# Optimization experiments

Measured on AMD Instinct MI355X. Metric: run time of the kernel, lower is better.

Reference implementation:

```python
import jax, jax.numpy as jnp
import numpy as np


def setup_inputs() -> dict:
    key = jax.random.key(0)
    ks = jax.random.split(key, 8)
    B, H, W, D, U = 128, 16, 48, 512, 512
    s = 1.0 / np.sqrt(D)
    return {
        "dec_hidden": jax.random.normal(ks[0], (B, D), jnp.float32),
        "enc_output": jax.random.normal(ks[1], (B, H, W, D), jnp.float32),
        "W1_w": jax.random.normal(ks[2], (D, U), jnp.float32) * s,
        "W1_b": jnp.zeros((U,), jnp.float32),
        "W2_w": jax.random.normal(ks[3], (D, U), jnp.float32) * s,
        "W2_b": jnp.zeros((U,), jnp.float32),
        "V_w": jax.random.normal(ks[4], (U, 1), jnp.float32) * (1.0 / np.sqrt(U)),
        "V_b": jnp.zeros((1,), jnp.float32),
    }


def reference(dec_hidden, enc_output, W1_w, W1_b, W2_w, W2_b, V_w, V_b):
    # dec_hidden: [B, Dd] -> [B, 1, 1, Dd]
    dec = dec_hidden[:, None, None, :]
    # W1(enc_output): [B, H, W, U]; W2(dec): [B, 1, 1, U] (broadcast add)
    h = jnp.tanh(jnp.einsum('bhwd,du->bhwu', enc_output, W1_w) + W1_b
                 + (dec @ W2_w + W2_b))
    # V(.) -> score [B, H, W, 1]
    score = jnp.einsum('bhwu,uo->bhwo', h, V_w) + V_b
    # softmax over axis=1 (H axis), matching tf.keras softmax(score, axis=1)
    attention_weights = jax.nn.softmax(score, axis=1)
    # context: sum over spatial axes -> [B, D]
    context_vector = jnp.sum(attention_weights * enc_output, axis=(1, 2))
    return context_vector, attention_weights
```

## Files before the change

kernel.cpp:

```cpp
#include <hip/hip_runtime.h>
#include <hip/hip_bf16.h>

typedef __attribute__((ext_vector_type(8))) short short8;
typedef __attribute__((ext_vector_type(4))) float f32x4;
typedef unsigned short ushort;

#define BB 128
#define HHH 16
#define WWW 48
#define DD 512
#define UU 512
#define ROWS_PER_B (HHH * WWW)
#define MTOT (BB * ROWS_PER_B)

__device__ __forceinline__ ushort f2bf(float f) {
    unsigned int u = __float_as_uint(f);
    u += 0x7fffu + ((u >> 16) & 1u);
    return (ushort)(u >> 16);
}

__device__ __forceinline__ void gload_lds16(const ushort* g, ushort* l) {
    __builtin_amdgcn_global_load_lds(
        (const __attribute__((address_space(1))) unsigned int*)(const void*)g,
        (__attribute__((address_space(3))) unsigned int*)(void*)l,
        16, 0, 0);
}

__global__ __launch_bounds__(256) void pack_w1p_kernel(const float* __restrict__ w1,
                                                       ushort* __restrict__ w1p) {
    __shared__ __align__(16) ushort tile[64 * 72];
    const int t  = threadIdx.x;
    const int u0 = blockIdx.x * 64;
    const int kc = blockIdx.y;
    const int ul = t & 63;
    const int db = t >> 6;
#pragma unroll
    for (int i = 0; i < 16; ++i) {
        const int d = db + i * 4;
        tile[ul * 72 + d] = f2bf(w1[(size_t)(kc * 64 + d) * UU + u0 + ul]);
    }
    __syncthreads();
    const int u = t >> 2;
    const int s = (t & 3) * 2;
    const int x = u & 7;
    short8 v0 = *(const short8*)&tile[u * 72 + s * 8];
    short8 v1 = *(const short8*)&tile[u * 72 + s * 8 + 8];
    *(short8*)&w1p[(size_t)kc * 32768 + (u0 + u) * 64 + (( s      ^ x)) * 8] = v0;
    *(short8*)&w1p[(size_t)kc * 32768 + (u0 + u) * 64 + (((s + 1) ^ x)) * 8] = v1;
}

__global__ __launch_bounds__(256) void dproj_kernel(
        const float* __restrict__ dec, const float* __restrict__ w2,
        const float* __restrict__ w1b, const float* __restrict__ w2b,
        float* __restrict__ dproj) {
    const int b = blockIdx.y;
    const int u = blockIdx.x * 256 + threadIdx.x;
    float acc = 0.f;
#pragma unroll 8
    for (int d = 0; d < DD; ++d)
        acc += dec[b * DD + d] * w2[(size_t)d * UU + u];
    dproj[b * UU + u] = acc + w1b[u] + w2b[u];
}

__global__ __launch_bounds__(512, 2) void score_kernel(
        const float* __restrict__ enc, const ushort* __restrict__ w1p,
        const float* __restrict__ dproj, const float* __restrict__ vw,
        const float* __restrict__ vb, float* __restrict__ score) {
    __shared__ __align__(16) ushort Bb[2][512 * 64];
    __shared__ __align__(16) ushort Ab[128 * 64];

    const int tid  = threadIdx.x;
    const int lane = tid & 63;
    const int wave = tid >> 6;
    const int mbase = blockIdx.x * 128;
    const int b = mbase / ROWS_PER_B;

    const int mh   = wave >> 2;
    const int uc   = wave & 3;
    const int lrow = lane & 15;
    const int kgrp = lane >> 4;

    const int ar  = tid >> 2;
    const int asp = (tid & 3) * 2;
    const float* abase = enc + (size_t)(mbase + ar) * DD + asp * 8;
    const int s0p = ( asp      ^ (ar & 7)) * 8;
    const int s1p = ((asp + 1) ^ (ar & 7)) * 8;

    f32x4 acc[4][8] = {};

    {
        float4 a0 = ((const float4*)abase)[0];
        float4 a1 = ((const float4*)abase)[1];
        float4 a2 = ((const float4*)abase)[2];
        float4 a3 = ((const float4*)abase)[3];
        const ushort* bsrc = w1p + tid * 8;
#pragma unroll
        for (int i = 0; i < 8; ++i)
            gload_lds16(bsrc + i * 4096, &Bb[0][tid * 8 + i * 4096]);
        short8 w0, w1v;
        ushort* p0 = (ushort*)&w0; ushort* p1 = (ushort*)&w1v;
        p0[0]=f2bf(a0.x); p0[1]=f2bf(a0.y); p0[2]=f2bf(a0.z); p0[3]=f2bf(a0.w);
        p0[4]=f2bf(a1.x); p0[5]=f2bf(a1.y); p0[6]=f2bf(a1.z); p0[7]=f2bf(a1.w);
        p1[0]=f2bf(a2.x); p1[1]=f2bf(a2.y); p1[2]=f2bf(a2.z); p1[3]=f2bf(a2.w);
        p1[4]=f2bf(a3.x); p1[5]=f2bf(a3.y); p1[6]=f2bf(a3.z); p1[7]=f2bf(a3.w);
        *(short8*)&Ab[ar * 64 + s0p] = w0;
        *(short8*)&Ab[ar * 64 + s1p] = w1v;
    }

    int cur = 0;
    for (int kc = 0; kc < 8; ++kc) {
        __syncthreads();

        float4 a0, a1, a2, a3;
        if (kc < 7) {
            const float* asrc = abase + (kc + 1) * 64;
            a0 = ((const float4*)asrc)[0];
            a1 = ((const float4*)asrc)[1];
            a2 = ((const float4*)asrc)[2];
            a3 = ((const float4*)asrc)[3];
            const ushort* bsrc = w1p + (size_t)(kc + 1) * 32768 + tid * 8;
#pragma unroll
            for (int i = 0; i < 8; ++i)
                gload_lds16(bsrc + i * 4096, &Bb[cur ^ 1][tid * 8 + i * 4096]);
        }

        const ushort* Bc = &Bb[cur][0];
#pragma unroll
        for (int kk = 0; kk < 2; ++kk) {
            const int sub = kk * 4 + kgrp;
            short8 a[4], bf[8];
#pragma unroll
            for (int ms = 0; ms < 4; ++ms) {
                const int r = mh * 64 + ms * 16 + lrow;
                a[ms] = *(const short8*)&Ab[r * 64 + (sub ^ (r & 7)) * 8];
            }
#pragma unroll
            for (int uf = 0; uf < 8; ++uf) {
                const int u = uc * 128 + uf * 16 + lrow;
                bf[uf] = *(const short8*)&Bc[u * 64 + (sub ^ (u & 7)) * 8];
            }
#pragma unroll
            for (int ms = 0; ms < 4; ++ms)
#pragma unroll
                for (int uf = 0; uf < 8; ++uf)
                    acc[ms][uf] = __builtin_amdgcn_mfma_f32_16x16x32_bf16(
                        a[ms], bf[uf], acc[ms][uf], 0, 0, 0);
        }

        __syncthreads();

        if (kc < 7) {
            short8 w0, w1v;
            ushort* p0 = (ushort*)&w0; ushort* p1 = (ushort*)&w1v;
            p0[0]=f2bf(a0.x); p0[1]=f2bf(a0.y); p0[2]=f2bf(a0.z); p0[3]=f2bf(a0.w);
            p0[4]=f2bf(a1.x); p0[5]=f2bf(a1.y); p0[6]=f2bf(a1.z); p0[7]=f2bf(a1.w);
            p1[0]=f2bf(a2.x); p1[1]=f2bf(a2.y); p1[2]=f2bf(a2.z); p1[3]=f2bf(a2.w);
            p1[4]=f2bf(a3.x); p1[5]=f2bf(a3.y); p1[6]=f2bf(a3.z); p1[7]=f2bf(a3.w);
            *(short8*)&Ab[ar * 64 + s0p] = w0;
            *(short8*)&Ab[ar * 64 + s1p] = w1v;
        }
        cur ^= 1;
    }

    float part[4][4] = {};
#pragma unroll
    for (int uf = 0; uf < 8; ++uf) {
        const int u = uc * 128 + uf * 16 + lrow;
        const float cadd = dproj[b * UU + u];
        const float vwe  = vw[u];
#pragma unroll
        for (int ms = 0; ms < 4; ++ms)
#pragma unroll
            for (int j = 0; j < 4; ++j) {
                float x = acc[ms][uf][j] + cadd;
                x = fminf(fmaxf(x, -15.f), 15.f);
                float e = __expf(2.f * x);
                part[ms][j] += vwe * ((e - 1.f) / (e + 1.f));
            }
    }
#pragma unroll
    for (int off = 1; off < 16; off <<= 1)
#pragma unroll
        for (int ms = 0; ms < 4; ++ms)
#pragma unroll
            for (int j = 0; j < 4; ++j)
                part[ms][j] += __shfl_xor(part[ms][j], off, 64);

    float* scr = (float*)Ab;
    if (lrow == 0) {
#pragma unroll
        for (int ms = 0; ms < 4; ++ms)
#pragma unroll
            for (int j = 0; j < 4; ++j)
                scr[uc * 128 + mh * 64 + ms * 16 + kgrp * 4 + j] = part[ms][j];
    }
    __syncthreads();
    if (tid < 128)
        score[mbase + tid] = scr[tid] + scr[128 + tid] + scr[256 + tid]
                           + scr[384 + tid] + vb[0];
}

__global__ void softmax_kernel(const float* __restrict__ score,
                               float* __restrict__ attn) {
    const int g = blockIdx.x * blockDim.x + threadIdx.x;
    if (g >= BB * WWW) return;
    const int b = g / WWW, w = g % WWW;
    const float* s = score + b * ROWS_PER_B + w;
    float v[16];
    float m = -1e30f;
#pragma unroll
    for (int h = 0; h < HHH; ++h) { v[h] = s[h * WWW]; m = fmaxf(m, v[h]); }
    float sum = 0.f;
#pragma unroll
    for (int h = 0; h < HHH; ++h) { v[h] = __expf(v[h] - m); sum += v[h]; }
    const float inv = 1.f / sum;
    float* o = attn + b * ROWS_PER_B + w;
#pragma unroll
    for (int h = 0; h < HHH; ++h) o[h * WWW] = v[h] * inv;
}

__global__ __launch_bounds__(512) void ctx_partial_kernel(
        const float* __restrict__ enc, const float* __restrict__ attn,
        float* __restrict__ partial) {
    const int c = blockIdx.x;
    const int b = blockIdx.y;
    const int t = threadIdx.x;
    const int d4 = (t & 127) * 4;
    const int ro = t >> 7;
    float4 acc = {0.f, 0.f, 0.f, 0.f};
    const int rbase = c * 192;
#pragma unroll 8
    for (int i = 0; i < 48; ++i) {
        const int r = rbase + ro + i * 4;
        const float a = attn[b * ROWS_PER_B + r];
        const float4 e = *(const float4*)(enc + ((size_t)(b * ROWS_PER_B + r)) * DD + d4);
        acc.x += a * e.x; acc.y += a * e.y; acc.z += a * e.z; acc.w += a * e.w;
    }
    *(float4*)(partial + ((size_t)((b * 4 + c) * 4 + ro)) * DD + d4) = acc;
}

__global__ void ctx_reduce_kernel(const float* __restrict__ partial,
                                  float* __restrict__ out) {
    const int q = blockIdx.x * 256 + threadIdx.x;
    const int b = q >> 7;
    const int d4 = (q & 127) * 4;
    float4 s = {0.f, 0.f, 0.f, 0.f};
#pragma unroll
    for (int j = 0; j < 16; ++j) {
        const float4 p = *(const float4*)(partial + ((size_t)(b * 16 + j)) * DD + d4);
        s.x += p.x; s.y += p.y; s.z += p.z; s.w += p.w;
    }
    *(float4*)(out + (size_t)b * DD + d4) = s;
}

extern "C" void kernel_launch(void* const* d_in, const int* in_sizes, int n_in,
                              void* d_out, int out_size, void* d_ws, size_t ws_size,
                              hipStream_t stream) {
    const float* dec = (const float*)d_in[0];
    const float* enc = (const float*)d_in[1];
    const float* w1w = (const float*)d_in[2];
    const float* w1b = (const float*)d_in[3];
    const float* w2w = (const float*)d_in[4];
    const float* w2b = (const float*)d_in[5];
    const float* vw  = (const float*)d_in[6];
    const float* vb  = (const float*)d_in[7];

    float* out = (float*)d_out;
    char* ws = (char*)d_ws;
    ushort* w1p    = (ushort*)(ws);
    float* dproj   = (float*)(ws + 524288);
    float* score   = (float*)(ws + 524288 + 262144);
    float* partial = (float*)(ws + 524288 + 262144 + 393216);

    float* ctx  = out;
    float* attn = out + BB * DD;

    pack_w1p_kernel<<<dim3(8, 8), 256, 0, stream>>>(w1w, w1p);
    dproj_kernel<<<dim3(2, BB), 256, 0, stream>>>(dec, w2w, w1b, w2b, dproj);
    score_kernel<<<MTOT / 128, 512, 0, stream>>>(enc, w1p, dproj, vw, vb, score);
    softmax_kernel<<<(BB * WWW + 255) / 256, 256, 0, stream>>>(score, attn);
    ctx_partial_kernel<<<dim3(4, BB), 512, 0, stream>>>(enc, attn, partial);
    ctx_reduce_kernel<<<64, 256, 0, stream>>>(partial, ctx);
}
```

Measured before the change: 409.0 us.

## Fuse prep and softmax kernels, double-buffer A tile to drop a barrier

Merges the W1 packing and decoder-projection kernels into one launch. Fuses the softmax into the context-partial kernel, which now recomputes softmax per batch from scores held in LDS and uses two row halves per batch instead of four. In the score GEMM, the A tile is double-buffered so the second __syncthreads per K step can be removed. This cuts launch overhead and barrier stalls, but raises LDS use to about 160KB per block and gives the context pass fewer blocks to work with.

```diff
diff --git a/kernel.cpp b/kernel.cpp
--- a/kernel.cpp
+++ b/kernel.cpp
@@ -26,48 +26,49 @@
         16, 0, 0);
 }
 
-__global__ __launch_bounds__(256) void pack_w1p_kernel(const float* __restrict__ w1,
-                                                       ushort* __restrict__ w1p) {
-    __shared__ __align__(16) ushort tile[64 * 72];
-    const int t  = threadIdx.x;
-    const int u0 = blockIdx.x * 64;
-    const int kc = blockIdx.y;
-    const int ul = t & 63;
-    const int db = t >> 6;
-#pragma unroll
-    for (int i = 0; i < 16; ++i) {
-        const int d = db + i * 4;
-        tile[ul * 72 + d] = f2bf(w1[(size_t)(kc * 64 + d) * UU + u0 + ul]);
-    }
-    __syncthreads();
-    const int u = t >> 2;
-    const int s = (t & 3) * 2;
-    const int x = u & 7;
-    short8 v0 = *(const short8*)&tile[u * 72 + s * 8];
-    short8 v1 = *(const short8*)&tile[u * 72 + s * 8 + 8];
-    *(short8*)&w1p[(size_t)kc * 32768 + (u0 + u) * 64 + (( s      ^ x)) * 8] = v0;
-    *(short8*)&w1p[(size_t)kc * 32768 + (u0 + u) * 64 + (((s + 1) ^ x)) * 8] = v1;
-}
-
-__global__ __launch_bounds__(256) void dproj_kernel(
-        const float* __restrict__ dec, const float* __restrict__ w2,
-        const float* __restrict__ w1b, const float* __restrict__ w2b,
-        float* __restrict__ dproj) {
-    const int b = blockIdx.y;
-    const int u = blockIdx.x * 256 + threadIdx.x;
-    float acc = 0.f;
+__global__ __launch_bounds__(256) void prep_kernel(
+        const float* __restrict__ w1, const float* __restrict__ dec,
+        const float* __restrict__ w2, const float* __restrict__ w1b,
+        const float* __restrict__ w2b,
+        ushort* __restrict__ w1p, float* __restrict__ dproj) {
+    const int t = threadIdx.x;
+    if (blockIdx.x < 64) {
+        __shared__ __align__(16) ushort tile[64 * 72];
+        const int u0 = (blockIdx.x & 7) * 64;
+        const int kc = blockIdx.x >> 3;
+        const int ul = t & 63;
+        const int db = t >> 6;
+#pragma unroll
+        for (int i = 0; i < 16; ++i) {
+            const int d = db + i * 4;
+            tile[ul * 72 + d] = f2bf(w1[(size_t)(kc * 64 + d) * UU + u0 + ul]);
+        }
+        __syncthreads();
+        const int u = t >> 2;
+        const int s = (t & 3) * 2;
+        const int x = u & 7;
+        short8 v0 = *(const short8*)&tile[u * 72 + s * 8];
+        short8 v1 = *(const short8*)&tile[u * 72 + s * 8 + 8];
+        *(short8*)&w1p[(size_t)kc * 32768 + (u0 + u) * 64 + (( s      ^ x)) * 8] = v0;
+        *(short8*)&w1p[(size_t)kc * 32768 + (u0 + u) * 64 + (((s + 1) ^ x)) * 8] = v1;
+    } else {
+        const int g = blockIdx.x - 64;
+        const int b = g >> 1;
+        const int u = (g & 1) * 256 + t;
+        float acc = 0.f;
 #pragma unroll 8
-    for (int d = 0; d < DD; ++d)
-        acc += dec[b * DD + d] * w2[(size_t)d * UU + u];
-    dproj[b * UU + u] = acc + w1b[u] + w2b[u];
+        for (int d = 0; d < DD; ++d)
+            acc += dec[b * DD + d] * w2[(size_t)d * UU + u];
+        dproj[b * UU + u] = acc + w1b[u] + w2b[u];
+    }
 }
 
 __global__ __launch_bounds__(512, 2) void score_kernel(
         const float* __restrict__ enc, const ushort* __restrict__ w1p,
         const float* __restrict__ dproj, const float* __restrict__ vw,
         const float* __restrict__ vb, float* __restrict__ score) {
-    __shared__ __align__(16) ushort Bb[2][512 * 64];
-    __shared__ __align__(16) ushort Ab[128 * 64];
+    __shared__ __align__(16) ushort Bb[2][UU * 64];
+    __shared__ __align__(16) ushort Ab[2][128 * 64];
 
     const int tid  = threadIdx.x;
     const int lane = tid & 63;
@@ -103,12 +104,13 @@
         p0[4]=f2bf(a1.x); p0[5]=f2bf(a1.y); p0[6]=f2bf(a1.z); p0[7]=f2bf(a1.w);
         p1[0]=f2bf(a2.x); p1[1]=f2bf(a2.y); p1[2]=f2bf(a2.z); p1[3]=f2bf(a2.w);
         p1[4]=f2bf(a3.x); p1[5]=f2bf(a3.y); p1[6]=f2bf(a3.z); p1[7]=f2bf(a3.w);
-        *(short8*)&Ab[ar * 64 + s0p] = w0;
-        *(short8*)&Ab[ar * 64 + s1p] = w1v;
-    }
-
-    int cur = 0;
+        *(short8*)&Ab[0][ar * 64 + s0p] = w0;
+        *(short8*)&Ab[0][ar * 64 + s1p] = w1v;
+    }
+
+#pragma unroll
     for (int kc = 0; kc < 8; ++kc) {
+        const int cur = kc & 1;
         __syncthreads();
 
         float4 a0, a1, a2, a3;
@@ -125,29 +127,28 @@
         }
 
         const ushort* Bc = &Bb[cur][0];
+        const ushort* Ac = &Ab[cur][0];
 #pragma unroll
         for (int kk = 0; kk < 2; ++kk) {
             const int sub = kk * 4 + kgrp;
-            short8 a[4], bf[8];
+            short8 afr[4], bfr[8];
 #pragma unroll
             for (int ms = 0; ms < 4; ++ms) {
                 const int r = mh * 64 + ms * 16 + lrow;
-                a[ms] = *(const short8*)&Ab[r * 64 + (sub ^ (r & 7)) * 8];
+                afr[ms] = *(const short8*)&Ac[r * 64 + (sub ^ (r & 7)) * 8];
             }
 #pragma unroll
             for (int uf = 0; uf < 8; ++uf) {
                 const int u = uc * 128 + uf * 16 + lrow;
-                bf[uf] = *(const short8*)&Bc[u * 64 + (sub ^ (u & 7)) * 8];
+                bfr[uf] = *(const short8*)&Bc[u * 64 + (sub ^ (u & 7)) * 8];
             }
 #pragma unroll
             for (int ms = 0; ms < 4; ++ms)
 #pragma unroll
                 for (int uf = 0; uf < 8; ++uf)
                     acc[ms][uf] = __builtin_amdgcn_mfma_f32_16x16x32_bf16(
-                        a[ms], bf[uf], acc[ms][uf], 0, 0, 0);
-        }
-
-        __syncthreads();
+                        afr[ms], bfr[uf], acc[ms][uf], 0, 0, 0);
+        }
 
         if (kc < 7) {
             short8 w0, w1v;
@@ -156,10 +157,9 @@
             p0[4]=f2bf(a1.x); p0[5]=f2bf(a1.y); p0[6]=f2bf(a1.z); p0[7]=f2bf(a1.w);
             p1[0]=f2bf(a2.x); p1[1]=f2bf(a2.y); p1[2]=f2bf(a2.z); p1[3]=f2bf(a2.w);
             p1[4]=f2bf(a3.x); p1[5]=f2bf(a3.y); p1[6]=f2bf(a3.z); p1[7]=f2bf(a3.w);
-            *(short8*)&Ab[ar * 64 + s0p] = w0;
-            *(short8*)&Ab[ar * 64 + s1p] = w1v;
-        }
-        cur ^= 1;
+            *(short8*)&Ab[cur ^ 1][ar * 64 + s0p] = w0;
+            *(short8*)&Ab[cur ^ 1][ar * 64 + s1p] = w1v;
+        }
     }
 
     float part[4][4] = {};
@@ -186,7 +186,7 @@
             for (int j = 0; j < 4; ++j)
                 part[ms][j] += __shfl_xor(part[ms][j], off, 64);
 
-    float* scr = (float*)Ab;
+    float* scr = (float*)&Ab[0][0];
     if (lrow == 0) {
 #pragma unroll
         for (int ms = 0; ms < 4; ++ms)
@@ -200,43 +200,48 @@
                            + scr[384 + tid] + vb[0];
 }
 
-__global__ void softmax_kernel(const float* __restrict__ score,
-                               float* __restrict__ attn) {
-    const int g = blockIdx.x * blockDim.x + threadIdx.x;
-    if (g >= BB * WWW) return;
-    const int b = g / WWW, w = g % WWW;
-    const float* s = score + b * ROWS_PER_B + w;
-    float v[16];
-    float m = -1e30f;
-#pragma unroll
-    for (int h = 0; h < HHH; ++h) { v[h] = s[h * WWW]; m = fmaxf(m, v[h]); }
-    float sum = 0.f;
-#pragma unroll
-    for (int h = 0; h < HHH; ++h) { v[h] = __expf(v[h] - m); sum += v[h]; }
-    const float inv = 1.f / sum;
-    float* o = attn + b * ROWS_PER_B + w;
-#pragma unroll
-    for (int h = 0; h < HHH; ++h) o[h * WWW] = v[h] * inv;
-}
-
-__global__ __launch_bounds__(512) void ctx_partial_kernel(
-        const float* __restrict__ enc, const float* __restrict__ attn,
-        float* __restrict__ partial) {
-    const int c = blockIdx.x;
-    const int b = blockIdx.y;
-    const int t = threadIdx.x;
+__global__ __launch_bounds__(512) void ctx_kernel(
+        const float* __restrict__ score, const float* __restrict__ enc,
+        float* __restrict__ attn, float* __restrict__ partial) {
+    __shared__ float sl[ROWS_PER_B];
+    __shared__ float al[ROWS_PER_B];
+    const int half = blockIdx.x;
+    const int b    = blockIdx.y;
+    const int t    = threadIdx.x;
+
+    for (int i = t; i < ROWS_PER_B; i += 512) sl[i] = score[b * ROWS_PER_B + i];
+    __syncthreads();
+
+    if (t < WWW) {
+        float v[HHH];
+        float m = -1e30f;
+#pragma unroll
+        for (int h = 0; h < HHH; ++h) { v[h] = sl[h * WWW + t]; m = fmaxf(m, v[h]); }
+        float sum = 0.f;
+#pragma unroll
+        for (int h = 0; h < HHH; ++h) { v[h] = __expf(v[h] - m); sum += v[h]; }
+        const float inv = 1.f / sum;
+#pragma unroll
+        for (int h = 0; h < HHH; ++h) al[h * WWW + t] = v[h] * inv;
+    }
+    __syncthreads();
+
+    const int rb = half * 384;
+    for (int i = t; i < 384; i += 512)
+        attn[b * ROWS_PER_B + rb + i] = al[rb + i];
+
+    const int r0 = t >> 7;
     const int d4 = (t & 127) * 4;
-    const int ro = t >> 7;
     float4 acc = {0.f, 0.f, 0.f, 0.f};
-    const int rbase = c * 192;
+    const float* ebase = enc + ((size_t)b * ROWS_PER_B + rb) * DD + d4;
 #pragma unroll 8
-    for (int i = 0; i < 48; ++i) {
-        const int r = rbase + ro + i * 4;
-        const float a = attn[b * ROWS_PER_B + r];
-        const float4 e = *(const float4*)(enc + ((size_t)(b * ROWS_PER_B + r)) * DD + d4);
+    for (int i = 0; i < 96; ++i) {
+        const int r = r0 + i * 4;
+        const float a = al[rb + r];
+        const float4 e = *(const float4*)(ebase + (size_t)r * DD);
         acc.x += a * e.x; acc.y += a * e.y; acc.z += a * e.z; acc.w += a * e.w;
     }
-    *(float4*)(partial + ((size_t)((b * 4 + c) * 4 + ro)) * DD + d4) = acc;
+    *(float4*)(partial + ((size_t)((b * 2 + half) * 4 + r0)) * DD + d4) = acc;
 }
 
 __global__ void ctx_reduce_kernel(const float* __restrict__ partial,
@@ -246,8 +251,8 @@
     const int d4 = (q & 127) * 4;
     float4 s = {0.f, 0.f, 0.f, 0.f};
 #pragma unroll
-    for (int j = 0; j < 16; ++j) {
-        const float4 p = *(const float4*)(partial + ((size_t)(b * 16 + j)) * DD + d4);
+    for (int j = 0; j < 8; ++j) {
+        const float4 p = *(const float4*)(partial + ((size_t)(b * 8 + j)) * DD + d4);
         s.x += p.x; s.y += p.y; s.z += p.z; s.w += p.w;
     }
     *(float4*)(out + (size_t)b * DD + d4) = s;
@@ -275,10 +280,8 @@
     float* ctx  = out;
     float* attn = out + BB * DD;
 
-    pack_w1p_kernel<<<dim3(8, 8), 256, 0, stream>>>(w1w, w1p);
-    dproj_kernel<<<dim3(2, BB), 256, 0, stream>>>(dec, w2w, w1b, w2b, dproj);
+    prep_kernel<<<320, 256, 0, stream>>>(w1w, dec, w2w, w1b, w2b, w1p, dproj);
     score_kernel<<<MTOT / 128, 512, 0, stream>>>(enc, w1p, dproj, vw, vb, score);
-    softmax_kernel<<<(BB * WWW + 255) / 256, 256, 0, stream>>>(score, attn);
-    ctx_partial_kernel<<<dim3(4, BB), 512, 0, stream>>>(enc, attn, partial);
+    ctx_kernel<<<dim3(2, BB), 512, 0, stream>>>(score, enc, attn, partial);
     ctx_reduce_kernel<<<64, 256, 0, stream>>>(partial, ctx);
 }
```

After: 417.3 us. 2.0% more time.
